# Optimization experiments

Measured on AMD Instinct MI355X. Metric: run time of the kernel, lower is better.

## Reference

```python
import jax, jax.numpy as jnp
import numpy as np

B, K, M = 8, 64, 128
Dg, Dn, De = 256, 256, 128
Hn, He = 512, 256
H, L = 8, 4
DH = Dn // H


def ln(x):
    m = x.mean(-1, keepdims=True)
    v = jnp.mean((x - m) ** 2, -1, keepdims=True)
    return (x - m) * jax.lax.rsqrt(v + 1e-5)


def setup_inputs() -> dict:
    key = jax.random.key(0)
    ks = iter(jax.random.split(key, 64))

    def rn(shape, scale=None):
        s = 1.0 / np.sqrt(shape[-2]) if scale is None else scale
        return jax.random.normal(next(ks), shape, dtype=jnp.float32) * s

    return {
        "graph_embedding": rn((B, K, Dg), 1.0),
        "Xq": rn((M, Dn), 0.02), "Eq": rn((M, M, De), 0.02),
        "Wq": rn((L, Dn, Dn)), "Wk": rn((L, Dg, Dn)), "Wv": rn((L, Dg, Dn)), "Wo": rn((L, Dn, Dn)),
        "Sq": rn((L, Dn, Dn)), "Sk": rn((L, Dn, Dn)), "Sv": rn((L, Dn, Dn)), "So": rn((L, Dn, Dn)),
        "Wb": rn((L, De, H)),
        "Wn1": rn((L, Dn, Hn)), "Wn2": rn((L, Hn, Dn)),
        "Woi": rn((L, Dn, De)), "Woj": rn((L, Dn, De)),
        "Wa": rn((L, De, De)), "Wga": rn((L, De, De)), "Wb2": rn((L, De, De)), "Wgb": rn((L, De, De)),
        "Wp": rn((L, De, De)), "Wgp": rn((L, De, De)),
        "We1": rn((L, De, He)), "We2": rn((L, He, De)),
        "hW": rn((Dn, 1)), "neW1": rn((Dn, Hn)), "neW2": rn((Hn, Dn)),
        "nlW": rn((Dn, 32)), "nfW1": rn((Dn, Hn)), "nfW2": rn((Hn, 16)),
        "aW": rn((De, 1)), "elW": rn((De, 8)), "efW1": rn((De, He)), "efW2": rn((He, 8)),
    }


def _decoder(graph_embedding, Xq, Eq, Wq, Wk, Wv, Wo, Sq, Sk, Sv, So, Wb,
             Wn1, Wn2, Woi, Woj, Wa, Wga, Wb2, Wgb, Wp, Wgp, We1, We2):
    X = jnp.broadcast_to(Xq, (B, M, Dn))          # learned node queries
    E = jnp.broadcast_to(Eq, (B, M, M, De))       # learned pair queries
    src = ln(graph_embedding)
    inv = 1.0 / np.sqrt(DH)
    for l in range(L):
        # cross-attention: nodes attend to graph-embedding tokens (pre-norm)
        Xn = ln(X)
        q = (Xn @ Wq[l]).reshape(B, M, H, DH)
        k = (src @ Wk[l]).reshape(B, K, H, DH)
        v = (src @ Wv[l]).reshape(B, K, H, DH)
        s = jnp.einsum('bmhd,bkhd->bhmk', q, k) * inv
        o = jnp.einsum('bhmk,bkhd->bmhd', jax.nn.softmax(s, -1), v).reshape(B, M, Dn)
        X = X + o @ Wo[l]
        # pair-biased node self-attention (AF2-style)
        Xn = ln(X)
        q = (Xn @ Sq[l]).reshape(B, M, H, DH)
        k = (Xn @ Sk[l]).reshape(B, M, H, DH)
        v = (Xn @ Sv[l]).reshape(B, M, H, DH)
        bias = jnp.einsum('bijc,ch->bhij', ln(E), Wb[l])
        s = jnp.einsum('bihd,bjhd->bhij', q, k) * inv + bias
        o = jnp.einsum('bhij,bjhd->bihd', jax.nn.softmax(s, -1), v).reshape(B, M, Dn)
        X = X + o @ So[l]
        # node transition MLP
        X = X + jax.nn.relu(ln(X) @ Wn1[l]) @ Wn2[l]
        # node -> edge outer-sum update
        Xn = ln(X)
        E = E + (Xn @ Woi[l])[:, :, None, :] + (Xn @ Woj[l])[:, None, :, :]
        # symmetric triangular multiplicative update  O(M^3 * De)
        En = ln(E)
        a = jax.nn.sigmoid(En @ Wga[l]) * (En @ Wa[l])
        b = jax.nn.sigmoid(En @ Wgb[l]) * (En @ Wb2[l])
        t = 0.5 * (jnp.einsum('bikc,bjkc->bijc', a, b)
                   + jnp.einsum('bkic,bkjc->bijc', a, b))
        E = E + jax.nn.sigmoid(En @ Wgp[l]) * (ln(t) @ Wp[l])
        # edge transition MLP
        E = E + jax.nn.relu(ln(E) @ We1[l]) @ We2[l]
    return ln(X), ln(E)


def reference(graph_embedding, Xq, Eq, Wq, Wk, Wv, Wo, Sq, Sk, Sv, So, Wb,
              Wn1, Wn2, Woi, Woj, Wa, Wga, Wb2, Wgb, Wp, Wgp, We1, We2,
              hW, neW1, neW2, nlW, nfW1, nfW2, aW, elW, efW1, efW2):
    X, E = _decoder(graph_embedding, Xq, Eq, Wq, Wk, Wv, Wo, Sq, Sk, Sv, So, Wb,
                    Wn1, Wn2, Woi, Woj, Wa, Wga, Wb2, Wgb, Wp, Wgp, We1, We2)
    h = (X @ hW)[..., 0]
    node_embeddings = jax.nn.relu(X @ neW1) @ neW2
    node_labels = X @ nlW
    node_features = jax.nn.relu(X @ nfW1) @ nfW2
    A = (E @ aW)[..., 0]
    edge_labels = E @ elW
    edge_features = jax.nn.relu(E @ efW1) @ efW2
    return (node_embeddings, h, node_labels, node_features, A, edge_labels, edge_features)
```

## Files before the change

kernel.cpp:

```cpp
#include <hip/hip_runtime.h>
#include <hip/hip_bf16.h>

using bf16 = __hip_bfloat16;

constexpr int Bc = 8, Kc = 64, Mc = 128, Dnc = 256, Dec = 128, Hnc = 512, Hec = 256, Hc = 8;
constexpr float INV_SQRT_DH = 0.17677669529663687f;

typedef __attribute__((ext_vector_type(8))) short s8v;
typedef __attribute__((ext_vector_type(4))) float f4v;
#define MFMA16(a, b, c) __builtin_amdgcn_mfma_f32_16x16x32_bf16(a, b, c, 0, 0, 0)

__device__ __forceinline__ float waveSum(float v) {
#pragma unroll
  for (int m = 32; m > 0; m >>= 1) v += __shfl_xor(v, m);
  return v;
}
__device__ __forceinline__ float b2f(unsigned short u) {
  union { unsigned x; float f; } v; v.x = (unsigned)u << 16; return v.f;
}
__device__ __forceinline__ unsigned short f2bu(float f) {
  bf16 h = __float2bfloat16(f); return *reinterpret_cast<unsigned short*>(&h);
}
__device__ __forceinline__ float ldf(const float* p) { return *p; }
__device__ __forceinline__ float ldf(const bf16* p)  { return __bfloat162float(*p); }
// ... 14 lines not shown
#pragma unroll
  for (int i = 0; i < NW; i++) tot += sb[i];
  float mean = tot * (1.0f / D);
  float d = v - mean;
  __syncthreads();
  float s2 = waveSum(d * d);
  if ((t & 63) == 0) sb[t >> 6] = s2;
  __syncthreads();
  float tot2 = 0.f;
#pragma unroll
  for (int i = 0; i < NW; i++) tot2 += sb[i];
  float rstd = rsqrtf(tot2 * (1.0f / D) + 1e-5f);
  stf(out + row * D + t, d * rstd);
}

template<typename InT, typename OutT>
__global__ __launch_bounds__(256) void ln128w_kernel(const InT* __restrict__ in,
                                                     OutT* __restrict__ out) {
  size_t row = (size_t)blockIdx.x * 4 + (threadIdx.x >> 6);
  int l = threadIdx.x & 63;
  const InT* p = in + row * 128 + l * 2;
  float v0 = ldf(p), v1 = ldf(p + 1);
  float mean = waveSum(v0 + v1) * (1.f / 128.f);
  float d0 = v0 - mean, d1 = v1 - mean;
  float rstd = rsqrtf(waveSum(d0 * d0 + d1 * d1) * (1.f / 128.f) + 1e-5f);
  OutT* q = out + row * 128 + l * 2;
  stf(q, d0 * rstd);
  stf(q + 1, d1 * rstd);
}

__global__ void bcast_kernel(const float* __restrict__ s, float* __restrict__ d,
                             unsigned mask, size_t total) {
  size_t i = (size_t)blockIdx.x * blockDim.x + threadIdx.x;
  if (i < total) d[i] = s[i & mask];
}

__global__ __launch_bounds__(256) void twcvt_kernel(const float* __restrict__ in,
                                                    bf16* __restrict__ out, int K, int N,
                                                    int inZ, int outZ) {
  const float* inp = in + (size_t)blockIdx.z * inZ;
  bf16* outp = out + (size_t)blockIdx.z * outZ;
  __shared__ float tile[32][33];
  int tx = threadIdx.x & 31, ty = threadIdx.x >> 5;
  int k0 = blockIdx.y * 32, n0 = blockIdx.x * 32;
#pragma unroll
  for (int it = 0; it < 4; it++)
    tile[ty + it * 8][tx] = inp[(size_t)(k0 + ty + it * 8) * N + n0 + tx];
  __syncthreads();
#pragma unroll
  for (int it = 0; it < 4; it++)
    outp[(size_t)(n0 + ty + it * 8) * K + k0 + tx] = __float2bfloat16(tile[tx][ty + it * 8]);
}

template<int ROWS>
__device__ __forceinline__ void stageTile(const bf16* __restrict__ g, int srcLd,
                                          char* lds, int t) {
  constexpr int IT = ROWS * 16 / 256;
#pragma unroll
  for (int it = 0; it < IT; it++) {
    int u = t + it * 256;
    int row = u >> 4, c16 = u & 15;
    uint4 val = *(const uint4*)(g + (size_t)row * srcLd + c16 * 8);
    *(uint4*)(lds + row * 256 + ((c16 ^ (row & 7)) << 4)) = val;
  }
}
__device__ __forceinline__ s8v readFrag(const char* lds, int row, int c16) {
  return *(const s8v*)(lds + row * 256 + ((c16 ^ (row & 7)) << 4));
}

template<int KTOT, int EPI>
__global__ __launch_bounds__(256) void ngemm128_kernel(
    const bf16* __restrict__ A, const bf16* __restrict__ Wt, void* __restrict__ outv,
    int N, int rowShift) {
  __shared__ char Ash[32768];
  __shared__ char Wsh[32768];
  int t = threadIdx.x, l = t & 63, w = t >> 6;
  size_t r0 = (size_t)blockIdx.x * 128;
  int c0 = blockIdx.y * 128;
  int rb = w * 32;
  f4v acc[2][8];
#pragma unroll
  for (int rf = 0; rf < 2; rf++)
#pragma unroll
    for (int cf = 0; cf < 8; cf++) acc[rf][cf] = (f4v){0.f, 0.f, 0.f, 0.f};
#pragma unroll
  for (int kb = 0; kb < KTOT; kb += 128) {
    if (kb) __syncthreads();
    stageTile<128>(A + r0 * KTOT + kb, KTOT, Ash, t);
    stageTile<128>(Wt + (size_t)c0 * KTOT + kb, KTOT, Wsh, t);
    __syncthreads();
#pragma unroll
    for (int kc = 0; kc < 4; kc++) {
      int c16 = kc * 4 + (l >> 4);
      s8v af[2];
#pragma unroll
      for (int rf = 0; rf < 2; rf++) af[rf] = readFrag(Ash, rb + rf * 16 + (l & 15), c16);
#pragma unroll
      for (int cf = 0; cf < 8; cf++) {
        s8v b0 = readFrag(Wsh, cf * 16 + (l & 15), c16);
#pragma unroll
        for (int rf = 0; rf < 2; rf++) acc[rf][cf] = MFMA16(af[rf], b0, acc[rf][cf]);
      }
    }
  }
#pragma unroll
  for (int rf = 0; rf < 2; rf++)
#pragma unroll
    for (int cf = 0; cf < 8; cf++)
#pragma unroll
      for (int i = 0; i < 4; i++) {
        size_t row = r0 + rb + rf * 16 + ((l >> 4) << 2) + i;
        int col = c0 + cf * 16 + (l & 15);
        float v = acc[rf][cf][i];
        if (EPI == 0) {
          ((float*)outv)[row * N + col] = v;
        } else if (EPI == 1) {
          ((bf16*)outv)[row * N + col] = __float2bfloat16(fmaxf(v, 0.f));
        } else {
          int seg = col >> 8, h = (col >> 5) & 7, d = col & 31;
          int b = (int)(row >> rowShift);
// ... 106 lines not shown
    const bf16* __restrict__ A, const bf16* __restrict__ Wt,
    float* __restrict__ X, bf16* __restrict__ Xnb) {
  __shared__ char Ash[16384];
  __shared__ char Wsh[65536];
  int t = threadIdx.x, l = t & 63, w = t >> 6;
  size_t r0 = (size_t)blockIdx.x * 64;
  int rb = w * 16;
  f4v acc[16];
#pragma unroll
  for (int cf = 0; cf < 16; cf++) acc[cf] = (f4v){0.f, 0.f, 0.f, 0.f};
#pragma unroll
  for (int kb = 0; kb < KTOT; kb += 128) {
    if (kb) __syncthreads();
    stageTile<64>(A + r0 * KTOT + kb, KTOT, Ash, t);
    stageTile<256>(Wt + kb, KTOT, Wsh, t);
    __syncthreads();
#pragma unroll
    for (int kc = 0; kc < 4; kc++) {
      int c16 = kc * 4 + (l >> 4);
      s8v af = readFrag(Ash, rb + (l & 15), c16);
#pragma unroll
      for (int cf = 0; cf < 16; cf++) {
        s8v b0 = readFrag(Wsh, cf * 16 + (l & 15), c16);
        acc[cf] = MFMA16(af, b0, acc[cf]);
      }
    }
  }
#pragma unroll
  for (int cf = 0; cf < 16; cf++)
#pragma unroll
    for (int i = 0; i < 4; i++) {
      size_t row = r0 + rb + ((l >> 4) << 2) + i;
      size_t o = row * 256 + cf * 16 + (l & 15);
      float e = X[o] + acc[cf][i];
      X[o] = e; acc[cf][i] = e;
    }
#pragma unroll
  for (int i = 0; i < 4; i++) {
    float s = 0.f, s2 = 0.f;
#pragma unroll
    for (int cf = 0; cf < 16; cf++) { float x = acc[cf][i]; s += x; s2 += x * x; }
#pragma unroll
    for (int m = 1; m < 16; m <<= 1) { s += __shfl_xor(s, m); s2 += __shfl_xor(s2, m); }
    float mean = s * 0.00390625f;
    float rstd = rsqrtf(s2 * 0.00390625f - mean * mean + 1e-5f);
    size_t row = r0 + rb + ((l >> 4) << 2) + i;
#pragma unroll
    for (int cf = 0; cf < 16; cf++)
      Xnb[row * 256 + cf * 16 + (l & 15)] = __float2bfloat16((acc[cf][i] - mean) * rstd);
  }
}

template<int EPI>
__global__ __launch_bounds__(256, 1) void mfma_nw2_kernel(
    const bf16* __restrict__ A, const bf16* __restrict__ W0t, const bf16* __restrict__ W1t,
    bf16* __restrict__ out) {
  __shared__ char lds[131072];
  char* Ash = lds; char* W0sh = lds + 65536; char* W1sh = lds + 98304;
  int t = threadIdx.x, l = t & 63, w = t >> 6;
  size_t r0 = (size_t)blockIdx.x * 256;
  int rb = w * 64;
  stageTile<256>(A + r0 * 128, 128, Ash, t);
  stageTile<128>(W0t, 128, W0sh, t);
  stageTile<128>(W1t, 128, W1sh, t);
  __syncthreads();
  f4v acc0[4][8], acc1[4][8];
#pragma unroll
  for (int rf = 0; rf < 4; rf++)
#pragma unroll
    for (int cf = 0; cf < 8; cf++) {
      acc0[rf][cf] = (f4v){0.f, 0.f, 0.f, 0.f};
      acc1[rf][cf] = (f4v){0.f, 0.f, 0.f, 0.f};
    }
#pragma unroll
  for (int kc = 0; kc < 4; kc++) {
    int c16 = kc * 4 + (l >> 4);
    s8v af[4];
#pragma unroll
    for (int rf = 0; rf < 4; rf++) af[rf] = readFrag(Ash, rb + rf * 16 + (l & 15), c16);
#pragma unroll
    for (int cf = 0; cf < 8; cf++) {
      s8v b0 = readFrag(W0sh, cf * 16 + (l & 15), c16);
      s8v b1 = readFrag(W1sh, cf * 16 + (l & 15), c16);
#pragma unroll
      for (int rf = 0; rf < 4; rf++) {
        acc0[rf][cf] = MFMA16(af[rf], b0, acc0[rf][cf]);
        acc1[rf][cf] = MFMA16(af[rf], b1, acc1[rf][cf]);
      }
    }
  }
  if (EPI == 1) {
#pragma unroll
    for (int rf = 0; rf < 4; rf++)
#pragma unroll
      for (int cf = 0; cf < 8; cf++)
#pragma unroll
        for (int i = 0; i < 4; i++) {
          size_t row = r0 + rb + rf * 16 + ((l >> 4) << 2) + i;
          int col = cf * 16 + (l & 15);
          out[row * 256 + col]       = __float2bfloat16(fmaxf(acc0[rf][cf][i], 0.f));
          out[row * 256 + 128 + col] = __float2bfloat16(fmaxf(acc1[rf][cf][i], 0.f));
        }
  } else {
    __syncthreads();
    char* tb = lds;
#pragma unroll
    for (int rf = 0; rf < 4; rf++)
#pragma unroll
      for (int cf = 0; cf < 8; cf++) {
        int c = cf * 16 + (l & 15);
        int u0 = rb + rf * 16 + ((l >> 4) << 2);
        uint2 pv;
        pv.x = (unsigned)f2bu(acc1[rf][cf][0] / (1.f + __expf(-acc0[rf][cf][0]))) |
               ((unsigned)f2bu(acc1[rf][cf][1] / (1.f + __expf(-acc0[rf][cf][1]))) << 16);
        pv.y = (unsigned)f2bu(acc1[rf][cf][2] / (1.f + __expf(-acc0[rf][cf][2]))) |
               ((unsigned)f2bu(acc1[rf][cf][3] / (1.f + __expf(-acc0[rf][cf][3]))) << 16);
        *(uint2*)(tb + c * 560 + u0 * 2) = pv;
      }
    __syncthreads();
    int b_ = (int)(r0 >> 14); int ik0 = (int)(r0 & 16383);
    bf16* op = out + (size_t)b_ * 2097152 + ik0;
#pragma unroll
    for (int q = 0; q < 16; q++) {
      int idx = q * 256 + t;
      int c = idx >> 5, li = idx & 31;
      *(uint4*)(op + (size_t)c * 16384 + li * 8) = *(const uint4*)(tb + c * 560 + li * 16);
    }
  }
}

__global__ __launch_bounds__(256, 1) void mfma_gmulsig_add_ln_kernel(
    const bf16* __restrict__ Tn, const bf16* __restrict__ Enin,
    const bf16* __restrict__ WpT, const bf16* __restrict__ WgpT,
    float* __restrict__ E, bf16* __restrict__ En) {
  __shared__ char lds[131072];
  char* Tsh = lds; char* Esh = lds + 32768; char* Wpsh = lds + 65536; char* Wgsh = lds + 98304;
  int t = threadIdx.x, l = t & 63, w = t >> 6;
  size_t r0 = (size_t)blockIdx.x * 128;
  int rb = w * 32;
  stageTile<128>(Tn + r0 * 128, 128, Tsh, t);
  stageTile<128>(Enin + r0 * 128, 128, Esh, t);
  stageTile<128>(WpT, 128, Wpsh, t);
  stageTile<128>(WgpT, 128, Wgsh, t);
  __syncthreads();
  f4v accp[2][8], accg[2][8];
#pragma unroll
  for (int rf = 0; rf < 2; rf++)
#pragma unroll
    for (int cf = 0; cf < 8; cf++) {
      accp[rf][cf] = (f4v){0.f, 0.f, 0.f, 0.f};
      accg[rf][cf] = (f4v){0.f, 0.f, 0.f, 0.f};
    }
#pragma unroll
  for (int kc = 0; kc < 4; kc++) {
    int c16 = kc * 4 + (l >> 4);
    s8v at[2], ae[2];
#pragma unroll
    for (int rf = 0; rf < 2; rf++) {
      at[rf] = readFrag(Tsh, rb + rf * 16 + (l & 15), c16);
      ae[rf] = readFrag(Esh, rb + rf * 16 + (l & 15), c16);
    }
#pragma unroll
    for (int cf = 0; cf < 8; cf++) {
      s8v bp = readFrag(Wpsh, cf * 16 + (l & 15), c16);
      s8v bg = readFrag(Wgsh, cf * 16 + (l & 15), c16);
#pragma unroll
      for (int rf = 0; rf < 2; rf++) {
        accp[rf][cf] = MFMA16(at[rf], bp, accp[rf][cf]);
        accg[rf][cf] = MFMA16(ae[rf], bg, accg[rf][cf]);
      }
    }
  }
#pragma unroll
  for (int rf = 0; rf < 2; rf++)
#pragma unroll
    for (int cf = 0; cf < 8; cf++)
#pragma unroll
      for (int i = 0; i < 4; i++) {
        size_t row = r0 + rb + rf * 16 + ((l >> 4) << 2) + i;
        size_t o = row * 128 + cf * 16 + (l & 15);
        float g = 1.f / (1.f + __expf(-accg[rf][cf][i]));
        float e = E[o] + g * accp[rf][cf][i];
        E[o] = e; accp[rf][cf][i] = e;
      }
#pragma unroll
  for (int rf = 0; rf < 2; rf++)
#pragma unroll
    for (int i = 0; i < 4; i++) {
      float s = 0.f, s2 = 0.f;
#pragma unroll
      for (int cf = 0; cf < 8; cf++) { float x = accp[rf][cf][i]; s += x; s2 += x * x; }
#pragma unroll
      for (int m = 1; m < 16; m <<= 1) { s += __shfl_xor(s, m); s2 += __shfl_xor(s2, m); }
      float mean = s * 0.0078125f;
      float rstd = rsqrtf(s2 * 0.0078125f - mean * mean + 1e-5f);
      size_t row = r0 + rb + rf * 16 + ((l >> 4) << 2) + i;
#pragma unroll
      for (int cf = 0; cf < 8; cf++)
        En[row * 128 + cf * 16 + (l & 15)] = __float2bfloat16((accp[rf][cf][i] - mean) * rstd);
    }
}

__global__ __launch_bounds__(256, 1) void mfma_mlp_ln_kernel(
    const bf16* __restrict__ Enin, const bf16* __restrict__ W1t, const bf16* __restrict__ W2t,
    float* __restrict__ E, bf16* __restrict__ En) {
  __shared__ char lds[131072];
  char* Ash = lds;
  char* W1sh = lds + 32768;
  char* Hs0 = lds + 65536;
  char* Hs1 = lds + 98304;
  int t = threadIdx.x, l = t & 63, w = t >> 6;
  size_t r0 = (size_t)blockIdx.x * 128;
  int rb = w * 32;
  stageTile<128>(Enin + r0 * 128, 128, Ash, t);
  stageTile<128>(W1t, 128, W1sh, t);
  __syncthreads();
#pragma unroll
  for (int half = 0; half < 2; half++) {
    if (half) {
      __syncthreads();
      stageTile<128>(W1t + 16384, 128, W1sh, t);
      __syncthreads();
    }
    f4v acc[2][8];
#pragma unroll
    for (int rf = 0; rf < 2; rf++)
#pragma unroll
      for (int cf = 0; cf < 8; cf++) acc[rf][cf] = (f4v){0.f, 0.f, 0.f, 0.f};
#pragma unroll
    for (int kc = 0; kc < 4; kc++) {
      int c16 = kc * 4 + (l >> 4);
      s8v af[2];
#pragma unroll
      for (int rf = 0; rf < 2; rf++) af[rf] = readFrag(Ash, rb + rf * 16 + (l & 15), c16);
#pragma unroll
      for (int cf = 0; cf < 8; cf++) {
        s8v b0 = readFrag(W1sh, cf * 16 + (l & 15), c16);
#pragma unroll
        for (int rf = 0; rf < 2; rf++) acc[rf][cf] = MFMA16(af[rf], b0, acc[rf][cf]);
      }
    }
    char* Hsh = half ? Hs1 : Hs0;
#pragma unroll
    for (int rf = 0; rf < 2; rf++)
#pragma unroll
      for (int cf = 0; cf < 8; cf++)
#pragma unroll
        for (int i = 0; i < 4; i++) {
          int row = rb + rf * 16 + ((l >> 4) << 2) + i;
          int col = cf * 16 + (l & 15);
          *(unsigned short*)(Hsh + row * 256 + (((col >> 3) ^ (row & 7)) << 4) + (col & 7) * 2)
              = f2bu(fmaxf(acc[rf][cf][i], 0.f));
        }
  }
  __syncthreads();
  stageTile<128>(W2t, 256, Ash, t);
  stageTile<128>(W2t + 128, 256, W1sh, t);
  __syncthreads();
  f4v acc2[2][8];
#pragma unroll
  for (int rf = 0; rf < 2; rf++)
#pragma unroll
    for (int cf = 0; cf < 8; cf++) acc2[rf][cf] = (f4v){0.f, 0.f, 0.f, 0.f};
#pragma unroll
  for (int kb = 0; kb < 2; kb++) {
    const char* Hb = kb ? Hs1 : Hs0;
    const char* Wb2 = kb ? W1sh : Ash;
#pragma unroll
    for (int kc = 0; kc < 4; kc++) {
      int c16 = kc * 4 + (l >> 4);
      s8v af[2];
#pragma unroll
      for (int rf = 0; rf < 2; rf++) af[rf] = readFrag(Hb, rb + rf * 16 + (l & 15), c16);
#pragma unroll
      for (int cf = 0; cf < 8; cf++) {
        s8v b0 = readFrag(Wb2, cf * 16 + (l & 15), c16);
#pragma unroll
        for (int rf = 0; rf < 2; rf++) acc2[rf][cf] = MFMA16(af[rf], b0, acc2[rf][cf]);
      }
    }
  }
#pragma unroll
  for (int rf = 0; rf < 2; rf++)
#pragma unroll
    for (int cf = 0; cf < 8; cf++)
#pragma unroll
      for (int i = 0; i < 4; i++) {
        size_t row = r0 + rb + rf * 16 + ((l >> 4) << 2) + i;
        size_t o = row * 128 + cf * 16 + (l & 15);
        float e = E[o] + acc2[rf][cf][i];
        E[o] = e; acc2[rf][cf][i] = e;
      }
#pragma unroll
  for (int rf = 0; rf < 2; rf++)
#pragma unroll
    for (int i = 0; i < 4; i++) {
      float s = 0.f, s2 = 0.f;
#pragma unroll
      for (int cf = 0; cf < 8; cf++) { float x = acc2[rf][cf][i]; s += x; s2 += x * x; }
#pragma unroll
      for (int m = 1; m < 16; m <<= 1) { s += __shfl_xor(s, m); s2 += __shfl_xor(s2, m); }
      float mean = s * 0.0078125f;
      float rstd = rsqrtf(s2 * 0.0078125f - mean * mean + 1e-5f);
      size_t row = r0 + rb + rf * 16 + ((l >> 4) << 2) + i;
#pragma unroll
      for (int cf = 0; cf < 8; cf++)
        En[row * 128 + cf * 16 + (l & 15)] = __float2bfloat16((acc2[rf][cf][i] - mean) * rstd);
    }
}

__global__ __launch_bounds__(256, 1) void tri_mfma_kernel(
    const bf16* __restrict__ aT, const bf16* __restrict__ bT, bf16* __restrict__ Tcm) {
  __shared__ char lds[131072];
  char* P1 = lds; char* Q1 = lds + 32768; char* P2 = lds + 65536; char* Q2 = lds + 98304;
  int t = threadIdx.x, l = t & 63, w = t >> 6;
  int bc = blockIdx.x;
  stageTile<128>(aT + (size_t)bc * 16384, 128, P1, t);
  stageTile<128>(bT + (size_t)bc * 16384, 128, Q1, t);
  __syncthreads();
#pragma unroll 8
  for (int it = 0; it < 64; it++) {
    int tile_ = w * 64 + it;
    int k0 = (tile_ & 15) * 8, r0 = (tile_ >> 4) * 8;
    int k = k0 + (l & 7), r = r0 + (l >> 3);
    int ra = r * 256 + ((((k >> 3) ^ (r & 7)) << 4)) + (k & 7) * 2;
    int wa = k * 256 + ((((r >> 3) ^ (k & 7)) << 4)) + (r & 7) * 2;
    *(unsigned short*)(P2 + wa) = *(const unsigned short*)(P1 + ra);
    *(unsigned short*)(Q2 + wa) = *(const unsigned short*)(Q1 + ra);
  }
  __syncthreads();
  int rb = w * 32;
  f4v acc1[2][8], acc2[2][8];
#pragma unroll
  for (int rf = 0; rf < 2; rf++)
#pragma unroll
    for (int cf = 0; cf < 8; cf++) {
      acc1[rf][cf] = (f4v){0.f, 0.f, 0.f, 0.f};
      acc2[rf][cf] = (f4v){0.f, 0.f, 0.f, 0.f};
    }
#pragma unroll
  for (int kc = 0; kc < 4; kc++) {
    int c16 = kc * 4 + (l >> 4);
    s8v a1[2], a2[2];
#pragma unroll
    for (int rf = 0; rf < 2; rf++) {
      a1[rf] = readFrag(P1, rb + rf * 16 + (l & 15), c16);
      a2[rf] = readFrag(P2, rb + rf * 16 + (l & 15), c16);
    }
#pragma unroll
    for (int cf = 0; cf < 8; cf++) {
      s8v b1 = readFrag(Q1, cf * 16 + (l & 15), c16);
      s8v b2 = readFrag(Q2, cf * 16 + (l & 15), c16);
#pragma unroll
      for (int rf = 0; rf < 2; rf++) {
        acc1[rf][cf] = MFMA16(a1[rf], b1, acc1[rf][cf]);
        acc2[rf][cf] = MFMA16(a2[rf], b2, acc2[rf][cf]);
      }
    }
  }
  __syncthreads();
  char* tb = lds;
#pragma unroll
  for (int rf = 0; rf < 2; rf++)
#pragma unroll
    for (int cf = 0; cf < 8; cf++) {
      int j = cf * 16 + (l & 15);
      int i0 = rb + rf * 16 + ((l >> 4) << 2);
      uint2 pv;
      pv.x = (unsigned)f2bu(0.5f * (acc1[rf][cf][0] + acc2[rf][cf][0])) |
             ((unsigned)f2bu(0.5f * (acc1[rf][cf][1] + acc2[rf][cf][1])) << 16);
      pv.y = (unsigned)f2bu(0.5f * (acc1[rf][cf][2] + acc2[rf][cf][2])) |
             ((unsigned)f2bu(0.5f * (acc1[rf][cf][3] + acc2[rf][cf][3])) << 16);
      *(uint2*)(tb + j * 560 + i0 * 2) = pv;
    }
  __syncthreads();
  bf16* op = Tcm + (size_t)bc * 16384;
#pragma unroll
  for (int q = 0; q < 8; q++) {
    int ci = q * 256 + t;
    *(uint4*)(op + ci * 8) = *(const uint4*)(tb + (ci >> 4) * 560 + (ci & 15) * 16);
  }
}

__global__ __launch_bounds__(256) void permln_kernel(const bf16* __restrict__ Tcm,
                                                     bf16* __restrict__ Tn) {
  __shared__ float tile[128][77];
  __shared__ float ps[4][64], ps2[4][64], mst[64], rst[64];
  int b = blockIdx.z, j = blockIdx.y, i0 = blockIdx.x * 64;
  int t = threadIdx.x;
  const bf16* src = Tcm + (size_t)b * 2097152 + j * 128 + i0;
#pragma unroll
  for (int q = 0; q < 4; q++) {
    int ci = q * 256 + t; int c = ci >> 3, ch = ci & 7;
    uint4 v = *(const uint4*)(src + (size_t)c * 16384 + ch * 8);
    const unsigned short* u = (const unsigned short*)&v;
#pragma unroll
    for (int e = 0; e < 8; e++) tile[c][ch * 8 + e] = b2f(u[e]);
  }
  __syncthreads();
  {
    int i_ = t & 63, part = t >> 6;
    float s = 0.f, s2 = 0.f;
    for (int c = part * 32; c < part * 32 + 32; c++) { float x = tile[c][i_]; s += x; s2 += x * x; }
    ps[part][i_] = s; ps2[part][i_] = s2;
  }
  __syncthreads();
  if (t < 64) {
    float s = ps[0][t] + ps[1][t] + ps[2][t] + ps[3][t];
    float q2 = ps2[0][t] + ps2[1][t] + ps2[2][t] + ps2[3][t];
    float mean = s * 0.0078125f;
    float var = q2 * 0.0078125f - mean * mean;
    mst[t] = mean; rst[t] = rsqrtf(var + 1e-5f);
  }
  __syncthreads();
  {
    int i2 = t & 63, c0 = (t >> 6) * 32;
    float mean = mst[i2], rstd = rst[i2];
    bf16* dst = Tn + ((size_t)b * 16384 + (size_t)(i0 + i2) * 128 + j) * 128 + c0;
#pragma unroll
    for (int qq = 0; qq < 4; qq++) {
      unsigned short pk[8];
#pragma unroll
      for (int e = 0; e < 8; e++)
        pk[e] = f2bu((tile[c0 + qq * 8 + e][i2] - mean) * rstd);
      *(uint4*)(dst + qq * 8) = *(uint4*)pk;
    }
  }
}

__global__ __launch_bounds__(256) void outer_ln_kernel(float* __restrict__ E,
    const float* __restrict__ xixj, bf16* __restrict__ En) {
  size_t r = (size_t)blockIdx.x * 4 + (threadIdx.x >> 6);
// ... 190 lines not shown
  twcvt_kernel<<<dim3(8, 8, 4), 256, 0, stream>>>(Wv, WkvT + 65536, 256, 256, 65536, 131072);
  twcvt_kernel<<<dim3(8, 8, 4), 256, 0, stream>>>(Sq, SqkvT, 256, 256, 65536, 196608);
  twcvt_kernel<<<dim3(8, 8, 4), 256, 0, stream>>>(Sk, SqkvT + 65536, 256, 256, 65536, 196608);
  twcvt_kernel<<<dim3(8, 8, 4), 256, 0, stream>>>(Sv, SqkvT + 131072, 256, 256, 65536, 196608);
  twcvt_kernel<<<dim3(8, 8, 4), 256, 0, stream>>>(Wo, WoT, 256, 256, 65536, 65536);
  twcvt_kernel<<<dim3(8, 8, 4), 256, 0, stream>>>(So, SoT, 256, 256, 65536, 65536);
  twcvt_kernel<<<dim3(16, 8, 4), 256, 0, stream>>>(Wn1, Wn1T, 256, 512, 131072, 131072);
  twcvt_kernel<<<dim3(8, 16, 4), 256, 0, stream>>>(Wn2, Wn2T, 512, 256, 131072, 131072);
  twcvt_kernel<<<dim3(4, 8, 4), 256, 0, stream>>>(Woi, WoijT, 256, 128, 32768, 65536);
  twcvt_kernel<<<dim3(4, 8, 4), 256, 0, stream>>>(Woj, WoijT + 32768, 256, 128, 32768, 65536);
  twcvt_kernel<<<dim3(16, 8, 1), 256, 0, stream>>>(neW1, neW1T, 256, 512, 131072, 131072);
  twcvt_kernel<<<dim3(8, 16, 1), 256, 0, stream>>>(neW2, neW2T, 512, 256, 131072, 131072);
  twcvt_kernel<<<dim3(16, 8, 1), 256, 0, stream>>>(nfW1, nfW1T, 256, 512, 131072, 131072);

  bcast_kernel<<<1024, 256, 0, stream>>>(Xq, X, 32767u, (size_t)262144);
  bcast_kernel<<<65536, 256, 0, stream>>>(Eq, E, 2097151u, (size_t)16777216);
  ln_kernel<256, float, bf16><<<1024, 256, 0, stream>>>(X, Xnb);
  ln_kernel<256, float, bf16><<<512, 256, 0, stream>>>(graph, srcb);
  ln128w_kernel<float, bf16><<<32768, 256, 0, stream>>>(E, En);

  for (int l = 0; l < 4; l++) {
    const bf16* WqT_l   = WqT   + l * 65536;
    const bf16* WkvT_l  = WkvT  + l * 131072;
    const bf16* SqkvT_l = SqkvT + l * 196608;
    const bf16* WoT_l   = WoT   + l * 65536;
    const bf16* SoT_l   = SoT   + l * 65536;
    const bf16* Wn1T_l  = Wn1T  + l * 131072;
    const bf16* Wn2T_l  = Wn2T  + l * 131072;
    const bf16* WoijT_l = WoijT + l * 65536;
    const float* Wb_l = Wb + l * 1024;
    const bf16* WgaT_l = WgaT + l * 16384; const bf16* WaT_l  = WaT  + l * 16384;
    const bf16* WgbT_l = WgbT + l * 16384; const bf16* Wb2T_l = Wb2T + l * 16384;
    const bf16* WgpT_l = WgpT + l * 16384; const bf16* WpT_l  = WpT  + l * 16384;
    const bf16* We1T_l = We1T + l * 32768; const bf16* We2T_l = We2T + l * 32768;

    ngemm128_kernel<256, 2><<<dim3(8, 2), 256, 0, stream>>>(Xnb, WqT_l, qb2, 256, 7);
    ngemm128_kernel<256, 2><<<dim3(4, 4), 256, 0, stream>>>(srcb, WkvT_l, kvb2, 512, 6);
    attn_mfma_kernel<64, 0><<<dim3(64, 2), 256, 0, stream>>>(
        qb2, kvb2, kvb2 + 131072, 2048, nullptr, obB);
    mfma_addx_ln_kernel<256><<<16, 256, 0, stream>>>(obB, WoT_l, X, Xnb);

    head8_kernel<128, 1, 0><<<4096, 256, 0, stream>>>(En, Wb_l, bias, nullptr, nullptr);
    ngemm128_kernel<256, 2><<<dim3(8, 6), 256, 0, stream>>>(Xnb, SqkvT_l, sqkvb, 768, 7);
    attn_mfma_kernel<128, 1><<<dim3(64, 2), 256, 0, stream>>>(
        sqkvb, sqkvb + 262144, sqkvb + 524288, 4096, bias, obB);
    mfma_addx_ln_kernel<256><<<16, 256, 0, stream>>>(obB, SoT_l, X, Xnb);

    ngemm128_kernel<256, 1><<<dim3(8, 4), 256, 0, stream>>>(Xnb, Wn1T_l, H1, 512, 0);
    mfma_addx_ln_kernel<512><<<16, 256, 0, stream>>>(H1, Wn2T_l, X, Xnb);

    ngemm128_kernel<256, 0><<<dim3(8, 2), 256, 0, stream>>>(Xnb, WoijT_l, xixj, 256, 0);
    outer_ln_kernel<<<32768, 256, 0, stream>>>(E, xixj, En);

    mfma_nw2_kernel<2><<<512, 256, 0, stream>>>(En, WgaT_l, WaT_l, aT1);
    mfma_nw2_kernel<2><<<512, 256, 0, stream>>>(En, WgbT_l, Wb2T_l, bT1);
    tri_mfma_kernel<<<1024, 256, 0, stream>>>(aT1, bT1, Tcm);
    permln_kernel<<<dim3(2, 128, 8), 256, 0, stream>>>(Tcm, Tn);
    mfma_gmulsig_add_ln_kernel<<<1024, 256, 0, stream>>>(Tn, En, WpT_l, WgpT_l, E, En);

    mfma_mlp_ln_kernel<<<1024, 256, 0, stream>>>(En, We1T_l, We2T_l, E, En);
  }

  ngemm128_kernel<256, 1><<<dim3(8, 4), 256, 0, stream>>>(Xnb, neW1T, H1, 512, 0);
  ngemm128_kernel<512, 0><<<dim3(8, 2), 256, 0, stream>>>(H1, neW2T, out_ne, 256, 0);
  rowdot_kernel<256, bf16><<<1024, 256, 0, stream>>>(Xnb, hW, out_h);
  headN_kernel<256, 32><<<128, 256, 0, stream>>>(Xnb, nlW, out_nl);
  ngemm128_kernel<256, 1><<<dim3(8, 4), 256, 0, stream>>>(Xnb, nfW1T, H1, 512, 0);
  headN_kernel<512, 16><<<64, 256, 0, stream>>>(H1, nfW2, out_nf);

  head8_kernel<128, 0, 1><<<4096, 256, 0, stream>>>(En, elW, out_el, aW, out_A);
  mfma_nw2_kernel<1><<<512, 256, 0, stream>>>(En, efW1T, efW1T + 16384, H);
  head8_kernel<256, 0, 0><<<4096, 256, 0, stream>>>(H, efW2, out_ef, nullptr, nullptr);
}
```

Measured before the change: 1.825 ms.

## Double wavefronts per block in edge-pair MFMA kernels to 512 threads

Five edge-path MFMA kernels (nw2, tri, gmulsig_add_ln, mlp_ln) go from 256 to 512 threads per block, each wave owning half as many rows, so per-wave accumulator arrays shrink. Because these kernels use 128KB of LDS and run one block per CU, the aim is more waves per CU to hide LDS and global latency. The hidden-activation LDS swizzle in the MLP kernel changes to XOR with row&15, and a matching fragment reader is added. In exchange each wave gets less reuse of the B fragments it reads from LDS, so LDS read traffic per MFMA roughly doubles.

Result: slower. 1.934 ms (+6.0%).

```diff
diff --git a/kernel.cpp b/kernel.cpp
--- a/kernel.cpp
+++ b/kernel.cpp
@@ -90,13 +90,13 @@
     outp[(size_t)(n0 + ty + it * 8) * K + k0 + tx] = __float2bfloat16(tile[tx][ty + it * 8]);
 }
 
-template<int ROWS>
+template<int ROWS, int NT = 256>
 __device__ __forceinline__ void stageTile(const bf16* __restrict__ g, int srcLd,
                                           char* lds, int t) {
-  constexpr int IT = ROWS * 16 / 256;
+  constexpr int IT = ROWS * 16 / NT;
 #pragma unroll
   for (int it = 0; it < IT; it++) {
-    int u = t + it * 256;
+    int u = t + it * NT;
     int row = u >> 4, c16 = u & 15;
     uint4 val = *(const uint4*)(g + (size_t)row * srcLd + c16 * 8);
     *(uint4*)(lds + row * 256 + ((c16 ^ (row & 7)) << 4)) = val;
@@ -104,6 +104,9 @@
 }
 __device__ __forceinline__ s8v readFrag(const char* lds, int row, int c16) {
   return *(const s8v*)(lds + row * 256 + ((c16 ^ (row & 7)) << 4));
+}
+__device__ __forceinline__ s8v readFragH(const char* lds, int row, int c16) {
+  return *(const s8v*)(lds + row * 256 + ((c16 ^ (row & 15)) << 4));
 }
 
 template<int KTOT, int EPI>
@@ -316,21 +319,21 @@
 }
 
 template<int EPI>
-__global__ __launch_bounds__(256, 1) void mfma_nw2_kernel(
+__global__ __launch_bounds__(512, 1) void mfma_nw2_kernel(
     const bf16* __restrict__ A, const bf16* __restrict__ W0t, const bf16* __restrict__ W1t,
     bf16* __restrict__ out) {
   __shared__ char lds[131072];
   char* Ash = lds; char* W0sh = lds + 65536; char* W1sh = lds + 98304;
   int t = threadIdx.x, l = t & 63, w = t >> 6;
   size_t r0 = (size_t)blockIdx.x * 256;
-  int rb = w * 64;
-  stageTile<256>(A + r0 * 128, 128, Ash, t);
-  stageTile<128>(W0t, 128, W0sh, t);
-  stageTile<128>(W1t, 128, W1sh, t);
-  __syncthreads();
-  f4v acc0[4][8], acc1[4][8];
-#pragma unroll
-  for (int rf = 0; rf < 4; rf++)
+  int rb = w * 32;
+  stageTile<256, 512>(A + r0 * 128, 128, Ash, t);
+  stageTile<128, 512>(W0t, 128, W0sh, t);
+  stageTile<128, 512>(W1t, 128, W1sh, t);
+  __syncthreads();
+  f4v acc0[2][8], acc1[2][8];
+#pragma unroll
+  for (int rf = 0; rf < 2; rf++)
 #pragma unroll
     for (int cf = 0; cf < 8; cf++) {
       acc0[rf][cf] = (f4v){0.f, 0.f, 0.f, 0.f};
@@ -339,15 +342,15 @@
 #pragma unroll
   for (int kc = 0; kc < 4; kc++) {
     int c16 = kc * 4 + (l >> 4);
-    s8v af[4];
-#pragma unroll
-    for (int rf = 0; rf < 4; rf++) af[rf] = readFrag(Ash, rb + rf * 16 + (l & 15), c16);
+    s8v af[2];
+#pragma unroll
+    for (int rf = 0; rf < 2; rf++) af[rf] = readFrag(Ash, rb + rf * 16 + (l & 15), c16);
 #pragma unroll
     for (int cf = 0; cf < 8; cf++) {
       s8v b0 = readFrag(W0sh, cf * 16 + (l & 15), c16);
       s8v b1 = readFrag(W1sh, cf * 16 + (l & 15), c16);
 #pragma unroll
-      for (int rf = 0; rf < 4; rf++) {
+      for (int rf = 0; rf < 2; rf++) {
         acc0[rf][cf] = MFMA16(af[rf], b0, acc0[rf][cf]);
         acc1[rf][cf] = MFMA16(af[rf], b1, acc1[rf][cf]);
       }
@@ -355,7 +358,7 @@
   }
   if (EPI == 1) {
 #pragma unroll
-    for (int rf = 0; rf < 4; rf++)
+    for (int rf = 0; rf < 2; rf++)
 #pragma unroll
       for (int cf = 0; cf < 8; cf++)
 #pragma unroll
@@ -369,7 +372,7 @@
     __syncthreads();
     char* tb = lds;
 #pragma unroll
-    for (int rf = 0; rf < 4; rf++)
+    for (int rf = 0; rf < 2; rf++)
 #pragma unroll
       for (int cf = 0; cf < 8; cf++) {
         int c = cf * 16 + (l & 15);
@@ -385,15 +388,15 @@
     int b_ = (int)(r0 >> 14); int ik0 = (int)(r0 & 16383);
     bf16* op = out + (size_t)b_ * 2097152 + ik0;
 #pragma unroll
-    for (int q = 0; q < 16; q++) {
-      int idx = q * 256 + t;
+    for (int q = 0; q < 8; q++) {
+      int idx = q * 512 + t;
       int c = idx >> 5, li = idx & 31;
       *(uint4*)(op + (size_t)c * 16384 + li * 8) = *(const uint4*)(tb + c * 560 + li * 16);
     }
   }
 }
 
-__global__ __launch_bounds__(256, 1) void mfma_gmulsig_add_ln_kernel(
+__global__ __launch_bounds__(512, 1) void mfma_gmulsig_add_ln_kernel(
     const bf16* __restrict__ Tn, const bf16* __restrict__ Enin,
     const bf16* __restrict__ WpT, const bf16* __restrict__ WgpT,
     float* __restrict__ E, bf16* __restrict__ En) {
@@ -401,71 +404,58 @@
   char* Tsh = lds; char* Esh = lds + 32768; char* Wpsh = lds + 65536; char* Wgsh = lds + 98304;
   int t = threadIdx.x, l = t & 63, w = t >> 6;
   size_t r0 = (size_t)blockIdx.x * 128;
-  int rb = w * 32;
-  stageTile<128>(Tn + r0 * 128, 128, Tsh, t);
-  stageTile<128>(Enin + r0 * 128, 128, Esh, t);
-  stageTile<128>(WpT, 128, Wpsh, t);
-  stageTile<128>(WgpT, 128, Wgsh, t);
-  __syncthreads();
-  f4v accp[2][8], accg[2][8];
-#pragma unroll
-  for (int rf = 0; rf < 2; rf++)
-#pragma unroll
-    for (int cf = 0; cf < 8; cf++) {
-      accp[rf][cf] = (f4v){0.f, 0.f, 0.f, 0.f};
-      accg[rf][cf] = (f4v){0.f, 0.f, 0.f, 0.f};
-    }
+  int rb = w * 16;
+  stageTile<128, 512>(Tn + r0 * 128, 128, Tsh, t);
+  stageTile<128, 512>(Enin + r0 * 128, 128, Esh, t);
+  stageTile<128, 512>(WpT, 128, Wpsh, t);
+  stageTile<128, 512>(WgpT, 128, Wgsh, t);
+  __syncthreads();
+  f4v accp[8], accg[8];
+#pragma unroll
+  for (int cf = 0; cf < 8; cf++) {
+    accp[cf] = (f4v){0.f, 0.f, 0.f, 0.f};
+    accg[cf] = (f4v){0.f, 0.f, 0.f, 0.f};
+  }
 #pragma unroll
   for (int kc = 0; kc < 4; kc++) {
     int c16 = kc * 4 + (l >> 4);
-    s8v at[2], ae[2];
-#pragma unroll
-    for (int rf = 0; rf < 2; rf++) {
-      at[rf] = readFrag(Tsh, rb + rf * 16 + (l & 15), c16);
-      ae[rf] = readFrag(Esh, rb + rf * 16 + (l & 15), c16);
-    }
+    s8v at = readFrag(Tsh, rb + (l & 15), c16);
+    s8v ae = readFrag(Esh, rb + (l & 15), c16);
 #pragma unroll
     for (int cf = 0; cf < 8; cf++) {
       s8v bp = readFrag(Wpsh, cf * 16 + (l & 15), c16);
       s8v bg = readFrag(Wgsh, cf * 16 + (l & 15), c16);
-#pragma unroll
-      for (int rf = 0; rf < 2; rf++) {
-        accp[rf][cf] = MFMA16(at[rf], bp, accp[rf][cf]);
-        accg[rf][cf] = MFMA16(ae[rf], bg, accg[rf][cf]);
-      }
-    }
-  }
-#pragma unroll
-  for (int rf = 0; rf < 2; rf++)
+      accp[cf] = MFMA16(at, bp, accp[cf]);
+      accg[cf] = MFMA16(ae, bg, accg[cf]);
+    }
+  }
+#pragma unroll
+  for (int cf = 0; cf < 8; cf++)
+#pragma unroll
+    for (int i = 0; i < 4; i++) {
+      size_t row = r0 + rb + ((l >> 4) << 2) + i;
+      size_t o = row * 128 + cf * 16 + (l & 15);
+      float g = 1.f / (1.f + __expf(-accg[cf][i]));
+      float e = E[o] + g * accp[cf][i];
+      E[o] = e; accp[cf][i] = e;
+    }
+#pragma unroll
+  for (int i = 0; i < 4; i++) {
+    float s = 0.f, s2 = 0.f;
+#pragma unroll
+    for (int cf = 0; cf < 8; cf++) { float x = accp[cf][i]; s += x; s2 += x * x; }
+#pragma unroll
+    for (int m = 1; m < 16; m <<= 1) { s += __shfl_xor(s, m); s2 += __shfl_xor(s2, m); }
+    float mean = s * 0.0078125f;
+    float rstd = rsqrtf(s2 * 0.0078125f - mean * mean + 1e-5f);
+    size_t row = r0 + rb + ((l >> 4) << 2) + i;
 #pragma unroll
     for (int cf = 0; cf < 8; cf++)
-#pragma unroll
-      for (int i = 0; i < 4; i++) {
-        size_t row = r0 + rb + rf * 16 + ((l >> 4) << 2) + i;
-        size_t o = row * 128 + cf * 16 + (l & 15);
-        float g = 1.f / (1.f + __expf(-accg[rf][cf][i]));
-        float e = E[o] + g * accp[rf][cf][i];
-        E[o] = e; accp[rf][cf][i] = e;
-      }
-#pragma unroll
-  for (int rf = 0; rf < 2; rf++)
-#pragma unroll
-    for (int i = 0; i < 4; i++) {
-      float s = 0.f, s2 = 0.f;
-#pragma unroll
-      for (int cf = 0; cf < 8; cf++) { float x = accp[rf][cf][i]; s += x; s2 += x * x; }
-#pragma unroll
-      for (int m = 1; m < 16; m <<= 1) { s += __shfl_xor(s, m); s2 += __shfl_xor(s2, m); }
-      float mean = s * 0.0078125f;
-      float rstd = rsqrtf(s2 * 0.0078125f - mean * mean + 1e-5f);
-      size_t row = r0 + rb + rf * 16 + ((l >> 4) << 2) + i;
-#pragma unroll
-      for (int cf = 0; cf < 8; cf++)
-        En[row * 128 + cf * 16 + (l & 15)] = __float2bfloat16((accp[rf][cf][i] - mean) * rstd);
-    }
-}
-
-__global__ __launch_bounds__(256, 1) void mfma_mlp_ln_kernel(
+      En[row * 128 + cf * 16 + (l & 15)] = __float2bfloat16((accp[cf][i] - mean) * rstd);
+  }
+}
+
+__global__ __launch_bounds__(512, 1) void mfma_mlp_ln_kernel(
     const bf16* __restrict__ Enin, const bf16* __restrict__ W1t, const bf16* __restrict__ W2t,
     float* __restrict__ E, bf16* __restrict__ En) {
   __shared__ char lds[131072];
@@ -475,57 +465,48 @@
   char* Hs1 = lds + 98304;
   int t = threadIdx.x, l = t & 63, w = t >> 6;
   size_t r0 = (size_t)blockIdx.x * 128;
-  int rb = w * 32;
-  stageTile<128>(Enin + r0 * 128, 128, Ash, t);
-  stageTile<128>(W1t, 128, W1sh, t);
+  int rb = w * 16;
+  stageTile<128, 512>(Enin + r0 * 128, 128, Ash, t);
+  stageTile<128, 512>(W1t, 128, W1sh, t);
   __syncthreads();
 #pragma unroll
   for (int half = 0; half < 2; half++) {
     if (half) {
       __syncthreads();
-      stageTile<128>(W1t + 16384, 128, W1sh, t);
+      stageTile<128, 512>(W1t + 16384, 128, W1sh, t);
       __syncthreads();
     }
-    f4v acc[2][8];
-#pragma unroll
-    for (int rf = 0; rf < 2; rf++)
-#pragma unroll
-      for (int cf = 0; cf < 8; cf++) acc[rf][cf] = (f4v){0.f, 0.f, 0.f, 0.f};
+    f4v acc[8];
+#pragma unroll
+    for (int cf = 0; cf < 8; cf++) acc[cf] = (f4v){0.f, 0.f, 0.f, 0.f};
 #pragma unroll
     for (int kc = 0; kc < 4; kc++) {
       int c16 = kc * 4 + (l >> 4);
-      s8v af[2];
-#pragma unroll
-      for (int rf = 0; rf < 2; rf++) af[rf] = readFrag(Ash, rb + rf * 16 + (l & 15), c16);
+      s8v af = readFrag(Ash, rb + (l & 15), c16);
 #pragma unroll
       for (int cf = 0; cf < 8; cf++) {
         s8v b0 = readFrag(W1sh, cf * 16 + (l & 15), c16);
-#pragma unroll
-        for (int rf = 0; rf < 2; rf++) acc[rf][cf] = MFMA16(af[rf], b0, acc[rf][cf]);
+        acc[cf] = MFMA16(af, b0, acc[cf]);
       }
     }
     char* Hsh = half ? Hs1 : Hs0;
 #pragma unroll
-    for (int rf = 0; rf < 2; rf++)
-#pragma unroll
-      for (int cf = 0; cf < 8; cf++)
-#pragma unroll
-        for (int i = 0; i < 4; i++) {
-          int row = rb + rf * 16 + ((l >> 4) << 2) + i;
-          int col = cf * 16 + (l & 15);
-          *(unsigned short*)(Hsh + row * 256 + (((col >> 3) ^ (row & 7)) << 4) + (col & 7) * 2)
-              = f2bu(fmaxf(acc[rf][cf][i], 0.f));
-        }
-  }
-  __syncthreads();
-  stageTile<128>(W2t, 256, Ash, t);
-  stageTile<128>(W2t + 128, 256, W1sh, t);
-  __syncthreads();
-  f4v acc2[2][8];
-#pragma unroll
-  for (int rf = 0; rf < 2; rf++)
-#pragma unroll
-    for (int cf = 0; cf < 8; cf++) acc2[rf][cf] = (f4v){0.f, 0.f, 0.f, 0.f};
+    for (int cf = 0; cf < 8; cf++)
+#pragma unroll
+      for (int i = 0; i < 4; i++) {
+        int row = rb + ((l >> 4) << 2) + i;
+        int col = cf * 16 + (l & 15);
+        *(unsigned short*)(Hsh + row * 256 + (((col >> 3) ^ (row & 15)) << 4) + (col & 7) * 2)
+            = f2bu(fmaxf(acc[cf][i], 0.f));
+      }
+  }
+  __syncthreads();
+  stageTile<128, 512>(W2t, 256, Ash, t);
+  stageTile<128, 512>(W2t + 128, 256, W1sh, t);
+  __syncthreads();
+  f4v acc2[8];
+#pragma unroll
+  for (int cf = 0; cf < 8; cf++) acc2[cf] = (f4v){0.f, 0.f, 0.f, 0.f};
 #pragma unroll
   for (int kb = 0; kb < 2; kb++) {
     const char* Hb = kb ? Hs1 : Hs0;
@@ -533,58 +514,51 @@
 #pragma unroll
     for (int kc = 0; kc < 4; kc++) {
       int c16 = kc * 4 + (l >> 4);
-      s8v af[2];
-#pragma unroll
-      for (int rf = 0; rf < 2; rf++) af[rf] = readFrag(Hb, rb + rf * 16 + (l & 15), c16);
+      s8v af = readFragH(Hb, rb + (l & 15), c16);
 #pragma unroll
       for (int cf = 0; cf < 8; cf++) {
         s8v b0 = readFrag(Wb2, cf * 16 + (l & 15), c16);
-#pragma unroll
-        for (int rf = 0; rf < 2; rf++) acc2[rf][cf] = MFMA16(af[rf], b0, acc2[rf][cf]);
+        acc2[cf] = MFMA16(af, b0, acc2[cf]);
       }
     }
   }
 #pragma unroll
-  for (int rf = 0; rf < 2; rf++)
+  for (int cf = 0; cf < 8; cf++)
+#pragma unroll
+    for (int i = 0; i < 4; i++) {
+      size_t row = r0 + rb + ((l >> 4) << 2) + i;
+      size_t o = row * 128 + cf * 16 + (l & 15);
+      float e = E[o] + acc2[cf][i];
+      E[o] = e; acc2[cf][i] = e;
+    }
+#pragma unroll
+  for (int i = 0; i < 4; i++) {
+    float s = 0.f, s2 = 0.f;
+#pragma unroll
+    for (int cf = 0; cf < 8; cf++) { float x = acc2[cf][i]; s += x; s2 += x * x; }
+#pragma unroll
+    for (int m = 1; m < 16; m <<= 1) { s += __shfl_xor(s, m); s2 += __shfl_xor(s2, m); }
+    float mean = s * 0.0078125f;
+    float rstd = rsqrtf(s2 * 0.0078125f - mean * mean + 1e-5f);
+    size_t row = r0 + rb + ((l >> 4) << 2) + i;
 #pragma unroll
     for (int cf = 0; cf < 8; cf++)
-#pragma unroll
-      for (int i = 0; i < 4; i++) {
-        size_t row = r0 + rb + rf * 16 + ((l >> 4) << 2) + i;
-        size_t o = row * 128 + cf * 16 + (l & 15);
-        float e = E[o] + acc2[rf][cf][i];
-        E[o] = e; acc2[rf][cf][i] = e;
-      }
-#pragma unroll
-  for (int rf = 0; rf < 2; rf++)
-#pragma unroll
-    for (int i = 0; i < 4; i++) {
-      float s = 0.f, s2 = 0.f;
-#pragma unroll
-      for (int cf = 0; cf < 8; cf++) { float x = acc2[rf][cf][i]; s += x; s2 += x * x; }
-#pragma unroll
-      for (int m = 1; m < 16; m <<= 1) { s += __shfl_xor(s, m); s2 += __shfl_xor(s2, m); }
-      float mean = s * 0.0078125f;
-      float rstd = rsqrtf(s2 * 0.0078125f - mean * mean + 1e-5f);
-      size_t row = r0 + rb + rf * 16 + ((l >> 4) << 2) + i;
-#pragma unroll
-      for (int cf = 0; cf < 8; cf++)
-        En[row * 128 + cf * 16 + (l & 15)] = __float2bfloat16((acc2[rf][cf][i] - mean) * rstd);
-    }
-}
-
-__global__ __launch_bounds__(256, 1) void tri_mfma_kernel(
+      En[row * 128 + cf * 16 + (l & 15)] = __float2bfloat16((acc2[cf][i] - mean) * rstd);
+  }
+}
+
+__global__ __launch_bounds__(512, 1) void tri_mfma_kernel(
     const bf16* __restrict__ aT, const bf16* __restrict__ bT, bf16* __restrict__ Tcm) {
   __shared__ char lds[131072];
   char* P1 = lds; char* Q1 = lds + 32768; char* P2 = lds + 65536; char* Q2 = lds + 98304;
   int t = threadIdx.x, l = t & 63, w = t >> 6;
   int bc = blockIdx.x;
-  stageTile<128>(aT + (size_t)bc * 16384, 128, P1, t);
-  stageTile<128>(bT + (size_t)bc * 16384, 128, Q1, t);
+  stageTile<128, 512>(aT + (size_t)bc * 16384, 128, P1, t);
+  stageTile<128, 512>(bT + (size_t)bc * 16384, 128, Q1, t);
   __syncthreads();
 #pragma unroll 8
-  for (int it = 0; it < 64; it++) {
-    int tile_ = w * 64 + it;
+  for (int it = 0; it < 32; it++) {
+    int tile_ = w * 32 + it;
     int k0 = (tile_ & 15) * 8, r0 = (tile_ >> 4) * 8;
     int k = k0 + (l & 7), r = r0 + (l >> 3);
     int ra = r * 256 + ((((k >> 3) ^ (r & 7)) << 4)) + (k & 7) * 2;
@@ -593,55 +567,44 @@
     *(unsigned short*)(Q2 + wa) = *(const unsigned short*)(Q1 + ra);
   }
   __syncthreads();
-  int rb = w * 32;
-  f4v acc1[2][8], acc2[2][8];
-#pragma unroll
-  for (int rf = 0; rf < 2; rf++)
-#pragma unroll
-    for (int cf = 0; cf < 8; cf++) {
-      acc1[rf][cf] = (f4v){0.f, 0.f, 0.f, 0.f};
-      acc2[rf][cf] = (f4v){0.f, 0.f, 0.f, 0.f};
-    }
+  int rb = w * 16;
+  f4v acc1[8], acc2[8];
+#pragma unroll
+  for (int cf = 0; cf < 8; cf++) {
+    acc1[cf] = (f4v){0.f, 0.f, 0.f, 0.f};
+    acc2[cf] = (f4v){0.f, 0.f, 0.f, 0.f};
+  }
 #pragma unroll
   for (int kc = 0; kc < 4; kc++) {
     int c16 = kc * 4 + (l >> 4);
-    s8v a1[2], a2[2];
-#pragma unroll
-    for (int rf = 0; rf < 2; rf++) {
-      a1[rf] = readFrag(P1, rb + rf * 16 + (l & 15), c16);
-      a2[rf] = readFrag(P2, rb + rf * 16 + (l & 15), c16);
-    }
+    s8v a1 = readFrag(P1, rb + (l & 15), c16);
+    s8v a2 = readFrag(P2, rb + (l & 15), c16);
 #pragma unroll
     for (int cf = 0; cf < 8; cf++) {
       s8v b1 = readFrag(Q1, cf * 16 + (l & 15), c16);
       s8v b2 = readFrag(Q2, cf * 16 + (l & 15), c16);
-#pragma unroll
-      for (int rf = 0; rf < 2; rf++) {
-        acc1[rf][cf] = MFMA16(a1[rf], b1, acc1[rf][cf]);
-        acc2[rf][cf] = MFMA16(a2[rf], b2, acc2[rf][cf]);
-      }
+      acc1[cf] = MFMA16(a1, b1, acc1[cf]);
+      acc2[cf] = MFMA16(a2, b2, acc2[cf]);
     }
   }
   __syncthreads();
   char* tb = lds;
 #pragma unroll
-  for (int rf = 0; rf < 2; rf++)
-#pragma unroll
-    for (int cf = 0; cf < 8; cf++) {
-      int j = cf * 16 + (l & 15);
-      int i0 = rb + rf * 16 + ((l >> 4) << 2);
-      uint2 pv;
-      pv.x = (unsigned)f2bu(0.5f * (acc1[rf][cf][0] + acc2[rf][cf][0])) |
-             ((unsigned)f2bu(0.5f * (acc1[rf][cf][1] + acc2[rf][cf][1])) << 16);
-      pv.y = (unsigned)f2bu(0.5f * (acc1[rf][cf][2] + acc2[rf][cf][2])) |
-             ((unsigned)f2bu(0.5f * (acc1[rf][cf][3] + acc2[rf][cf][3])) << 16);
-      *(uint2*)(tb + j * 560 + i0 * 2) = pv;
-    }
+  for (int cf = 0; cf < 8; cf++) {
+    int j = cf * 16 + (l & 15);
+    int i0 = rb + ((l >> 4) << 2);
+    uint2 pv;
+    pv.x = (unsigned)f2bu(0.5f * (acc1[cf][0] + acc2[cf][0])) |
+           ((unsigned)f2bu(0.5f * (acc1[cf][1] + acc2[cf][1])) << 16);
+    pv.y = (unsigned)f2bu(0.5f * (acc1[cf][2] + acc2[cf][2])) |
+           ((unsigned)f2bu(0.5f * (acc1[cf][3] + acc2[cf][3])) << 16);
+    *(uint2*)(tb + j * 560 + i0 * 2) = pv;
+  }
   __syncthreads();
   bf16* op = Tcm + (size_t)bc * 16384;
 #pragma unroll
-  for (int q = 0; q < 8; q++) {
-    int ci = q * 256 + t;
+  for (int q = 0; q < 4; q++) {
+    int ci = q * 512 + t;
     *(uint4*)(op + ci * 8) = *(const uint4*)(tb + (ci >> 4) * 560 + (ci & 15) * 16);
   }
 }
@@ -938,13 +901,13 @@
     ngemm128_kernel<256, 0><<<dim3(8, 2), 256, 0, stream>>>(Xnb, WoijT_l, xixj, 256, 0);
     outer_ln_kernel<<<32768, 256, 0, stream>>>(E, xixj, En);
 
-    mfma_nw2_kernel<2><<<512, 256, 0, stream>>>(En, WgaT_l, WaT_l, aT1);
-    mfma_nw2_kernel<2><<<512, 256, 0, stream>>>(En, WgbT_l, Wb2T_l, bT1);
-    tri_mfma_kernel<<<1024, 256, 0, stream>>>(aT1, bT1, Tcm);
+    mfma_nw2_kernel<2><<<512, 512, 0, stream>>>(En, WgaT_l, WaT_l, aT1);
+    mfma_nw2_kernel<2><<<512, 512, 0, stream>>>(En, WgbT_l, Wb2T_l, bT1);
+    tri_mfma_kernel<<<1024, 512, 0, stream>>>(aT1, bT1, Tcm);
     permln_kernel<<<dim3(2, 128, 8), 256, 0, stream>>>(Tcm, Tn);
-    mfma_gmulsig_add_ln_kernel<<<1024, 256, 0, stream>>>(Tn, En, WpT_l, WgpT_l, E, En);
-
-    mfma_mlp_ln_kernel<<<1024, 256, 0, stream>>>(En, We1T_l, We2T_l, E, En);
+    mfma_gmulsig_add_ln_kernel<<<1024, 512, 0, stream>>>(Tn, En, WpT_l, WgpT_l, E, En);
+
+    mfma_mlp_ln_kernel<<<1024, 512, 0, stream>>>(En, We1T_l, We2T_l, E, En);
   }
 
   ngemm128_kernel<256, 1><<<dim3(8, 4), 256, 0, stream>>>(Xnb, neW1T, H1, 512, 0);
@@ -955,6 +918,6 @@
   headN_kernel<512, 16><<<64, 256, 0, stream>>>(H1, nfW2, out_nf);
 
   head8_kernel<128, 0, 1><<<4096, 256, 0, stream>>>(En, elW, out_el, aW, out_A);
-  mfma_nw2_kernel<1><<<512, 256, 0, stream>>>(En, efW1T, efW1T + 16384, H);
+  mfma_nw2_kernel<1><<<512, 512, 0, stream>>>(En, efW1T, efW1T + 16384, H);
   head8_kernel<256, 0, 0><<<4096, 256, 0, stream>>>(H, efW2, out_ef, nullptr, nullptr);
 }
```
